# Performance work log

Measured on AMD Instinct MI355X. Metric: run time of the kernel, lower is better.

Reference implementation:

```python
import jax, jax.numpy as jnp
import numpy as np

N_NODES = 384
IN_F = 128
HID = 256
NUM_RBF = 50
NUM_BASIS = 8
NUM_HEADS = 8
HEAD_D = HID // NUM_HEADS
INT_OUT = 2 * NUM_RBF * NUM_BASIS            # K and Q, each num_rbf*num_basis
NODE_OUT = NUM_BASIS * NUM_BASIS + 2 * NUM_BASIS  # W0, B0, W1


def setup_inputs() -> dict:
    key = jax.random.key(0)
    ks = jax.random.split(key, 13)
    s = 0.05
    def p(k, shape):
        return jax.random.normal(k, shape, jnp.float32) * s
    return {
        "h": jax.random.normal(ks[0], (N_NODES, IN_F), jnp.float32),
        "fc_w": p(ks[1], (HID, IN_F)),
        "fc_b": p(ks[2], (HID,)),
        "in_proj_w": p(ks[3], (3 * HID, HID)),
        "in_proj_b": p(ks[4], (3 * HID,)),
        "out_proj_w": p(ks[5], (HID, HID)),
        "out_proj_b": p(ks[6], (HID,)),
        "fci_w1": p(ks[7], (HID, 2 * HID)),
        "fci_b1": p(ks[8], (HID,)),
        "fci_w2": p(ks[9], (INT_OUT, HID)),
        "fci_b2": p(ks[10], (INT_OUT,)),
        "fcn_w": p(ks[11], (NODE_OUT, HID)),
        "fcn_b": p(ks[12], (NODE_OUT,)),
    }


def reference(h, fc_w, fc_b, in_proj_w, in_proj_b, out_proj_w, out_proj_b,
              fci_w1, fci_b1, fci_w2, fci_b2, fcn_w, fcn_b):
    n = h.shape[0]
    # input projection
    h = h @ fc_w.T + fc_b                                   # (n, HID)
    # multihead self-attention (torch nn.MultiheadAttention math)
    qkv = h @ in_proj_w.T + in_proj_b                       # (n, 3*HID)
    q, k, v = jnp.split(qkv, 3, axis=-1)
    def heads(x):
        return x.reshape(n, NUM_HEADS, HEAD_D).transpose(1, 0, 2)  # (H, n, D)
    q, k, v = heads(q), heads(k), heads(v)
    scores = jnp.einsum('hnd,hmd->hnm', q, k) / jnp.sqrt(jnp.asarray(HEAD_D, h.dtype))
    attn = jax.nn.softmax(scores, axis=-1)
    h = jnp.einsum('hnm,hmd->hnd', attn, v).transpose(1, 0, 2).reshape(n, HID)
    h = h @ out_proj_w.T + out_proj_b                       # (n, HID)
    # pairwise interaction: h_interaction[i, j] = concat(h[j], h[i])
    # first Linear split algebraically: cat(hj, hi) @ W1.T = hj@Wa.T + hi@Wb.T
    wa, wb = fci_w1[:, :HID], fci_w1[:, HID:]
    pre = (h @ wa.T)[None, :, :] + (h @ wb.T)[:, None, :] + fci_b1  # (n, n, HID)
    kq = jnp.tanh(pre) @ fci_w2.T + fci_b2                  # (n, n, INT_OUT)
    K, Q = jnp.split(kq, 2, axis=-1)
    K = K.reshape(n, n, NUM_RBF, NUM_BASIS)
    Q = Q.reshape(n, n, NUM_RBF, NUM_BASIS)
    # node-wise parameters
    node = h @ fcn_w.T + fcn_b                              # (n, NODE_OUT)
    b2 = NUM_BASIS * NUM_BASIS
    W0 = node[:, :b2].reshape(n, NUM_BASIS, NUM_BASIS)
    B0 = node[:, b2:b2 + NUM_BASIS]
    W1 = node[:, b2 + NUM_BASIS:].reshape(n, NUM_BASIS, 1)
    return (K, Q, W0, B0, W1)
```

## Files before the change

### kernel.cpp

```cpp
#include <hip/hip_runtime.h>
#include <hip/hip_bf16.h>

typedef __attribute__((ext_vector_type(8))) short bf16x8;
typedef __attribute__((ext_vector_type(4))) float f32x4;

static __device__ __forceinline__ unsigned int f2bf(float f) {
    unsigned int u = __float_as_uint(f);
    u = u + 0x7FFFu + ((u >> 16) & 1u);
    return (u >> 16);
}

static __device__ __forceinline__ float fast_tanh(float x) {
    x = fminf(fmaxf(x, -10.f), 10.f);
    float e = __expf(2.f * x);
    return __fdividef(e - 1.f, e + 1.f);
}

#define LGKM_BAR() do {                                      \
    asm volatile("s_waitcnt lgkmcnt(0)" ::: "memory");       \
    __builtin_amdgcn_s_barrier();                            \
} while (0)

#define LGKM_WAIT() asm volatile("s_waitcnt lgkmcnt(0)" ::: "memory")

__global__ __launch_bounds__(256)
void prep(const float* __restrict__ fc_w, const float* __restrict__ inp_w,
          const float* __restrict__ outp_w, const float* __restrict__ fci_w1,
          const float* __restrict__ fcn_w, const float* __restrict__ fci_w2,
          float* __restrict__ fcwT, float* __restrict__ inpT,
          float* __restrict__ outpT, float* __restrict__ waT,
          float* __restrict__ wbT, float* __restrict__ fcnT,
          uint4* __restrict__ w2p)
{
    const int idx0 = blockIdx.x * 256 + threadIdx.x;
    const int stride = 64 * 256;
    switch (blockIdx.y) {
    case 0:
        for (int c = idx0; c < 32768; c += stride) {
            int k = c >> 8, n = c & 255;
            fcwT[c] = fc_w[n * 128 + k];
        }
        break;
    case 1:
        for (int c = idx0; c < 196608; c += stride) {
            int k = c / 768, n = c - k * 768;
            inpT[c] = inp_w[n * 256 + k];
        }
        break;
    case 2:
        for (int c = idx0; c < 65536; c += stride) {
            int k = c >> 8, n = c & 255;
            outpT[c] = outp_w[n * 256 + k];
        }
        break;
    case 3:
        for (int c = idx0; c < 65536; c += stride) {
            int k = c >> 8, n = c & 255;
            waT[c] = fci_w1[n * 512 + k];
        }
        break;
    case 4:
        for (int c = idx0; c < 65536; c += stride) {
            int k = c >> 8, n = c & 255;
            wbT[c] = fci_w1[n * 512 + 256 + k];
        }
        break;
    case 5:
        for (int c = idx0; c < 20480; c += stride) {
            int k = c / 80, n = c - k * 80;
            fcnT[c] = fcn_w[n * 256 + k];
        }
        break;
    default:
        for (int c = idx0; c < 25600; c += stride) {
            const int n_g = c >> 5, e = c & 31;
            const int kk = e >> 2, kg = e & 3;
            const int ph = (n_g >= 400) ? 1 : 0;
            const int n = n_g - ph * 400;
            const float4* s = (const float4*)(fci_w2 + n_g * 256 + kk * 32 + kg * 8);
            const float4 x0 = s[0], x1 = s[1];
            uint4 pk;
            pk.x = f2bf(x0.x) | (f2bf(x0.y) << 16);
            pk.y = f2bf(x0.z) | (f2bf(x0.w) << 16);
            pk.z = f2bf(x1.x) | (f2bf(x1.y) << 16);
            pk.w = f2bf(x1.z) | (f2bf(x1.w) << 16);
            w2p[((ph * 8 + kk) * 400 + n) * 4 + kg] = pk;
        }
        break;
    }
}

__global__ __launch_bounds__(256)
void k1_rows(const float* __restrict__ h, const float* __restrict__ fc_b,
             const float* __restrict__ inp_b, const float* __restrict__ fcwT,
             const float* __restrict__ inpT, float* __restrict__ qkv)
{
    __shared__ float hrow[128];
    __shared__ float h1row[256];
    const int i = blockIdx.x, part = blockIdx.y, tid = threadIdx.x;
    if (tid < 128) hrow[tid] = h[i * 128 + tid];
    __syncthreads();
    float acc = fc_b[tid];
    #pragma unroll 8
    for (int k = 0; k < 128; ++k) acc += hrow[k] * fcwT[k * 256 + tid];
    h1row[tid] = acc;
    __syncthreads();
    const int col = part * 256 + tid;
    float a = inp_b[col];
    #pragma unroll 8
    for (int k = 0; k < 256; ++k) a += h1row[k] * inpT[k * 768 + col];
    qkv[i * 768 + col] = a;
}

__global__ __launch_bounds__(256)
void attn_kernel(const float* __restrict__ qkv, float* __restrict__ out)
{
    const int n = blockIdx.x;
    const int h = blockIdx.y;
    const int tid = threadIdx.x;
    const int lane = tid & 63;
    const int wid = tid >> 6;

    __shared__ float qs[32];
    __shared__ float p[384];
    __shared__ float red[8];
    __shared__ float pv[8][32];

    if (tid < 32) qs[tid] = qkv[n * 768 + h * 32 + tid] * 0.17677669529663687f;
    __syncthreads();

    float lmax = -1e30f;
    for (int m = tid; m < 384; m += 256) {
        const float4* kr = (const float4*)(qkv + m * 768 + 256 + h * 32);
        float s = 0.f;
        #pragma unroll
        for (int d = 0; d < 8; ++d) {
            float4 kv = kr[d];
            s += qs[d*4+0]*kv.x + qs[d*4+1]*kv.y + qs[d*4+2]*kv.z + qs[d*4+3]*kv.w;
        }
        p[m] = s;
        lmax = fmaxf(lmax, s);
    }
    #pragma unroll
    for (int off = 32; off >= 1; off >>= 1) lmax = fmaxf(lmax, __shfl_xor(lmax, off));
    if (lane == 0) red[wid] = lmax;
    __syncthreads();
    const float gmax = fmaxf(fmaxf(red[0], red[1]), fmaxf(red[2], red[3]));

    float lsum = 0.f;
    for (int m = tid; m < 384; m += 256) {
        float e = __expf(p[m] - gmax);
        p[m] = e;
        lsum += e;
    }
    #pragma unroll
    for (int off = 32; off >= 1; off >>= 1) lsum += __shfl_xor(lsum, off);
    if (lane == 0) red[4 + wid] = lsum;
    __syncthreads();
    const float inv = 1.f / (red[4] + red[5] + red[6] + red[7]);

    const int d = tid & 31;
    const int g = tid >> 5;
    float acc = 0.f;
    for (int m = g * 48; m < g * 48 + 48; ++m)
        acc += p[m] * qkv[m * 768 + 512 + h * 32 + d];
    pv[g][d] = acc;
    __syncthreads();
    if (tid < 32) {
        float o = 0.f;
        #pragma unroll
        for (int gg = 0; gg < 8; ++gg) o += pv[gg][tid];
        out[n * 256 + h * 32 + tid] = o * inv;
    }
}

__global__ __launch_bounds__(256)
void k3_rows(const float* __restrict__ attnO, const float* __restrict__ outp_b,
             const float* __restrict__ fci_b1, const float* __restrict__ fcn_b,
             const float* __restrict__ outpT, const float* __restrict__ waT,
             const float* __restrict__ wbT, const float* __restrict__ fcnT,
             float* __restrict__ hA, float* __restrict__ hB, float* __restrict__ out)
{
    __shared__ float arow[256];
    __shared__ float h2row[256];
    const int i = blockIdx.x, part = blockIdx.y, tid = threadIdx.x;
    arow[tid] = attnO[i * 256 + tid];
    __syncthreads();
    float acc = outp_b[tid];
    #pragma unroll 8
    for (int k = 0; k < 256; ++k) acc += arow[k] * outpT[k * 256 + tid];
    h2row[tid] = acc;
    __syncthreads();
    if (part == 0) {
        float aA = fci_b1[tid];
        #pragma unroll 8
        for (int k = 0; k < 256; ++k) aA += h2row[k] * waT[k * 256 + tid];
        hA[i * 256 + tid] = aA;
    } else if (part == 1) {
        float aB = 0.f;
        #pragma unroll 8
        for (int k = 0; k < 256; ++k) aB += h2row[k] * wbT[k * 256 + tid];
        hB[i * 256 + tid] = aB;
    } else if (tid < 80) {
        float aN = fcn_b[tid];
        #pragma unroll 8
        for (int k = 0; k < 256; ++k) aN += h2row[k] * fcnT[k * 80 + tid];
        if (tid < 64)      out[117964800 + i * 64 + tid] = aN;
        else if (tid < 72) out[117989376 + i * 8 + (tid - 64)] = aN;
        else               out[117992448 + i * 8 + (tid - 72)] = aN;
    }
}

#define CSW_ROWB 336

__global__ __launch_bounds__(320)
void gen_kq(const float* __restrict__ hA, const float* __restrict__ hB,
            const uint4* __restrict__ w2p, const float* __restrict__ b2,
            float* __restrict__ outK, float* __restrict__ outQ)
{
    __shared__ unsigned char Aim[48 * 512];
    __shared__ unsigned char Csw[5][16 * CSW_ROWB];

    const int tid  = threadIdx.x;
    const int lane = tid & 63;
    const int wn   = tid >> 6;
    const int lr   = lane & 15;
    const int kg   = lane >> 4;

    const int bid0 = blockIdx.x;
    const int bid  = (bid0 & 7) * 384 + (bid0 >> 3);

    const int m0  = bid * 48;
    const int ai  = bid >> 3;
    const int bj0 = (bid & 7) * 48;

    for (int c = tid; c < 1536; c += 320) {
        const int row = c >> 5;
        const int e   = c & 31;
        const int ke  = e * 8;
        const float4 a0 = *(const float4*)(hA + (bj0 + row) * 256 + ke);
        const float4 a1 = *(const float4*)(hA + (bj0 + row) * 256 + ke + 4);
        const float4 b0 = *(const float4*)(hB + ai * 256 + ke);
        const float4 b1 = *(const float4*)(hB + ai * 256 + ke + 4);
        uint4 pk;
        pk.x = f2bf(fast_tanh(a0.x + b0.x)) | (f2bf(fast_tanh(a0.y + b0.y)) << 16);
        pk.y = f2bf(fast_tanh(a0.z + b0.z)) | (f2bf(fast_tanh(a0.w + b0.w)) << 16);
        pk.z = f2bf(fast_tanh(a1.x + b1.x)) | (f2bf(fast_tanh(a1.y + b1.y)) << 16);
        pk.w = f2bf(fast_tanh(a1.z + b1.z)) | (f2bf(fast_tanh(a1.w + b1.w)) << 16);
        *(uint4*)(Aim + row * 512 + ((e * 16) ^ ((row & 7) << 4))) = pk;
    }
    LGKM_BAR();

    const int phfirst = bid & 1;
    #pragma unroll
    for (int pp = 0; pp < 2; ++pp) {
        const int ph = pp ^ phfirst;

        f32x4 acc[3][5];
        #pragma unroll
        for (int j = 0; j < 5; ++j) {
            const f32x4 bb = *(const f32x4*)(b2 + ph * 400 + wn * 80 + j * 16 + kg * 4);
            #pragma unroll
            for (int i = 0; i < 3; ++i)
                acc[i][j] = bb;
        }

        #pragma unroll 2
        for (int kk = 0; kk < 8; ++kk) {
            bf16x8 af_[3], bf_[5];
            const uint4* wb = w2p + (ph * 8 + kk) * 1600;
            #pragma unroll
            for (int j = 0; j < 5; ++j)
                bf_[j] = *(const bf16x8*)(wb + (wn * 80 + j * 16 + lr) * 4 + kg);
            #pragma unroll
            for (int i = 0; i < 3; ++i) {
                const int row = i * 16 + lr;
                af_[i] = *(const bf16x8*)(Aim + row * 512 +
                          ((kk * 64 + kg * 16) ^ ((row & 7) << 4)));
            }
            #pragma unroll
            for (int i = 0; i < 3; ++i)
                #pragma unroll
                for (int j = 0; j < 5; ++j)
                    acc[i][j] = __builtin_amdgcn_mfma_f32_16x16x32_bf16(
                        bf_[j], af_[i], acc[i][j], 0, 0, 0);
        }

        float* gob = ph ? outQ : outK;
        unsigned char* slice = Csw[wn];
        #pragma unroll
        for (int i = 0; i < 3; ++i) {
            #pragma unroll
            for (int j = 0; j < 5; ++j)
                *(f32x4*)(slice + lr * CSW_ROWB + (j * 16 + kg * 4) * 4) = acc[i][j];
            LGKM_WAIT();
            float* gb = gob + (size_t)(m0 + i * 16) * 400 + wn * 80;
            #pragma unroll
            for (int q = 0; q < 5; ++q) {
                const int e   = q * 64 + lane;
                const int row = e / 20, c4 = e - row * 20;
                const f32x4 v = *(const f32x4*)(slice + row * CSW_ROWB + c4 * 16);
                *(f32x4*)(gb + row * 400 + c4 * 4) = v;
            }
        }
    }
}

extern "C" void kernel_launch(void* const* d_in, const int* in_sizes, int n_in,
                              void* d_out, int out_size, void* d_ws, size_t ws_size,
                              hipStream_t stream)
{
    (void)in_sizes; (void)n_in; (void)out_size; (void)ws_size;

    const float* h      = (const float*)d_in[0];
    const float* fc_w   = (const float*)d_in[1];
    const float* fc_b   = (const float*)d_in[2];
    const float* inp_w  = (const float*)d_in[3];
    const float* inp_b  = (const float*)d_in[4];
    const float* outp_w = (const float*)d_in[5];
    const float* outp_b = (const float*)d_in[6];
    const float* fci_w1 = (const float*)d_in[7];
    const float* fci_b1 = (const float*)d_in[8];
    const float* fci_w2 = (const float*)d_in[9];
    const float* fci_b2 = (const float*)d_in[10];
    const float* fcn_w  = (const float*)d_in[11];
    const float* fcn_b  = (const float*)d_in[12];

    float* out  = (float*)d_out;
    float* outK = out;
    float* outQ = out + 58982400;

    float* ws    = (float*)d_ws;
    float* qkv   = ws;
    float* attnO = qkv   + 294912;
    float* hA    = attnO + 98304;
    float* hBv   = hA    + 98304;
    float* fcwT  = hBv   + 98304;
    float* inpT  = fcwT  + 32768;
    float* outpT = inpT  + 196608;
    float* waT   = outpT + 65536;
    float* wbT   = waT   + 65536;
    float* fcnT  = wbT   + 65536;
    uint4* w2p   = (uint4*)(fcnT + 20480);

    prep<<<dim3(64, 7), 256, 0, stream>>>(fc_w, inp_w, outp_w, fci_w1, fcn_w, fci_w2,
                                          fcwT, inpT, outpT, waT, wbT, fcnT, w2p);
    k1_rows<<<dim3(384, 3), 256, 0, stream>>>(h, fc_b, inp_b, fcwT, inpT, qkv);
    attn_kernel<<<dim3(384, 8), 256, 0, stream>>>(qkv, attnO);
    k3_rows<<<dim3(384, 3), 256, 0, stream>>>(attnO, outp_b, fci_b1, fcn_b, outpT, waT, wbT, fcnT,
                                              hA, hBv, out);
    gen_kq<<<dim3(3072), 320, 0, stream>>>(hA, hBv, w2p, fci_b2, outK, outQ);
}
```

Measured before the change: 222.1 us.

## Fuse weight prep into k1 and merge attention with output projections

Drops the separate weight-transpose prep kernel, so the small linear layers read the original row-major weights directly, and folds the bf16 packing of fci_w2 into extra blocks of the first kernel. The attention kernel now handles all eight heads for one node per block and also computes the out projection and the fci/fcn projections, cutting five launches down to three and removing the attnO round trip. The trade-off is strided, uncoalesced weight reads per thread, and far fewer blocks (384) in the fused attention stage, each doing serial per-head work.

```diff
diff --git a/kernel.cpp b/kernel.cpp
--- a/kernel.cpp
+++ b/kernel.cpp
@@ -24,55 +24,15 @@
 #define LGKM_WAIT() asm volatile("s_waitcnt lgkmcnt(0)" ::: "memory")
 
 __global__ __launch_bounds__(256)
-void prep(const float* __restrict__ fc_w, const float* __restrict__ inp_w,
-          const float* __restrict__ outp_w, const float* __restrict__ fci_w1,
-          const float* __restrict__ fcn_w, const float* __restrict__ fci_w2,
-          float* __restrict__ fcwT, float* __restrict__ inpT,
-          float* __restrict__ outpT, float* __restrict__ waT,
-          float* __restrict__ wbT, float* __restrict__ fcnT,
-          uint4* __restrict__ w2p)
-{
-    const int idx0 = blockIdx.x * 256 + threadIdx.x;
-    const int stride = 64 * 256;
-    switch (blockIdx.y) {
-    case 0:
-        for (int c = idx0; c < 32768; c += stride) {
-            int k = c >> 8, n = c & 255;
-            fcwT[c] = fc_w[n * 128 + k];
-        }
-        break;
-    case 1:
-        for (int c = idx0; c < 196608; c += stride) {
-            int k = c / 768, n = c - k * 768;
-            inpT[c] = inp_w[n * 256 + k];
-        }
-        break;
-    case 2:
-        for (int c = idx0; c < 65536; c += stride) {
-            int k = c >> 8, n = c & 255;
-            outpT[c] = outp_w[n * 256 + k];
-        }
-        break;
-    case 3:
-        for (int c = idx0; c < 65536; c += stride) {
-            int k = c >> 8, n = c & 255;
-            waT[c] = fci_w1[n * 512 + k];
-        }
-        break;
-    case 4:
-        for (int c = idx0; c < 65536; c += stride) {
-            int k = c >> 8, n = c & 255;
-            wbT[c] = fci_w1[n * 512 + 256 + k];
-        }
-        break;
-    case 5:
-        for (int c = idx0; c < 20480; c += stride) {
-            int k = c / 80, n = c - k * 80;
-            fcnT[c] = fcn_w[n * 256 + k];
-        }
-        break;
-    default:
-        for (int c = idx0; c < 25600; c += stride) {
+void k1_all(const float* __restrict__ h, const float* __restrict__ fc_b,
+            const float* __restrict__ inp_b, const float* __restrict__ fc_w,
+            const float* __restrict__ inp_w, const float* __restrict__ fci_w2,
+            float* __restrict__ qkv, uint4* __restrict__ w2p)
+{
+    const int i = blockIdx.x, part = blockIdx.y, tid = threadIdx.x;
+    if (part == 3) {
+        const int c = i * 256 + tid;
+        if (c < 25600) {
             const int n_g = c >> 5, e = c & 31;
             const int kk = e >> 2, kg = e & 3;
             const int ph = (n_g >= 400) ? 1 : 0;
@@ -86,125 +46,118 @@
             pk.w = f2bf(x1.z) | (f2bf(x1.w) << 16);
             w2p[((ph * 8 + kk) * 400 + n) * 4 + kg] = pk;
         }
-        break;
-    }
-}
-
-__global__ __launch_bounds__(256)
-void k1_rows(const float* __restrict__ h, const float* __restrict__ fc_b,
-             const float* __restrict__ inp_b, const float* __restrict__ fcwT,
-             const float* __restrict__ inpT, float* __restrict__ qkv)
-{
+        return;
+    }
     __shared__ float hrow[128];
     __shared__ float h1row[256];
-    const int i = blockIdx.x, part = blockIdx.y, tid = threadIdx.x;
     if (tid < 128) hrow[tid] = h[i * 128 + tid];
     __syncthreads();
     float acc = fc_b[tid];
-    #pragma unroll 8
-    for (int k = 0; k < 128; ++k) acc += hrow[k] * fcwT[k * 256 + tid];
+    const float* fwr = fc_w + tid * 128;
+    #pragma unroll 8
+    for (int k = 0; k < 128; ++k) acc += hrow[k] * fwr[k];
     h1row[tid] = acc;
     __syncthreads();
     const int col = part * 256 + tid;
     float a = inp_b[col];
-    #pragma unroll 8
-    for (int k = 0; k < 256; ++k) a += h1row[k] * inpT[k * 768 + col];
+    const float* iwr = inp_w + (long)col * 256;
+    #pragma unroll 8
+    for (int k = 0; k < 256; ++k) a += h1row[k] * iwr[k];
     qkv[i * 768 + col] = a;
 }
 
 __global__ __launch_bounds__(256)
-void attn_kernel(const float* __restrict__ qkv, float* __restrict__ out)
-{
-    const int n = blockIdx.x;
-    const int h = blockIdx.y;
+void attn_k3(const float* __restrict__ qkv, const float* __restrict__ outp_b,
+             const float* __restrict__ fci_b1, const float* __restrict__ fcn_b,
+             const float* __restrict__ outp_w, const float* __restrict__ fci_w1,
+             const float* __restrict__ fcn_w,
+             float* __restrict__ hA, float* __restrict__ hB, float* __restrict__ out)
+{
+    const int i = blockIdx.x;
     const int tid = threadIdx.x;
     const int lane = tid & 63;
     const int wid = tid >> 6;
 
-    __shared__ float qs[32];
+    __shared__ float qs[256];
     __shared__ float p[384];
     __shared__ float red[8];
     __shared__ float pv[8][32];
-
-    if (tid < 32) qs[tid] = qkv[n * 768 + h * 32 + tid] * 0.17677669529663687f;
-    __syncthreads();
-
-    float lmax = -1e30f;
-    for (int m = tid; m < 384; m += 256) {
-        const float4* kr = (const float4*)(qkv + m * 768 + 256 + h * 32);
-        float s = 0.f;
-        #pragma unroll
-        for (int d = 0; d < 8; ++d) {
-            float4 kv = kr[d];
-            s += qs[d*4+0]*kv.x + qs[d*4+1]*kv.y + qs[d*4+2]*kv.z + qs[d*4+3]*kv.w;
-        }
-        p[m] = s;
-        lmax = fmaxf(lmax, s);
-    }
-    #pragma unroll
-    for (int off = 32; off >= 1; off >>= 1) lmax = fmaxf(lmax, __shfl_xor(lmax, off));
-    if (lane == 0) red[wid] = lmax;
-    __syncthreads();
-    const float gmax = fmaxf(fmaxf(red[0], red[1]), fmaxf(red[2], red[3]));
-
-    float lsum = 0.f;
-    for (int m = tid; m < 384; m += 256) {
-        float e = __expf(p[m] - gmax);
-        p[m] = e;
-        lsum += e;
-    }
-    #pragma unroll
-    for (int off = 32; off >= 1; off >>= 1) lsum += __shfl_xor(lsum, off);
-    if (lane == 0) red[4 + wid] = lsum;
-    __syncthreads();
-    const float inv = 1.f / (red[4] + red[5] + red[6] + red[7]);
-
-    const int d = tid & 31;
-    const int g = tid >> 5;
-    float acc = 0.f;
-    for (int m = g * 48; m < g * 48 + 48; ++m)
-        acc += p[m] * qkv[m * 768 + 512 + h * 32 + d];
-    pv[g][d] = acc;
-    __syncthreads();
-    if (tid < 32) {
-        float o = 0.f;
-        #pragma unroll
-        for (int gg = 0; gg < 8; ++gg) o += pv[gg][tid];
-        out[n * 256 + h * 32 + tid] = o * inv;
-    }
-}
-
-__global__ __launch_bounds__(256)
-void k3_rows(const float* __restrict__ attnO, const float* __restrict__ outp_b,
-             const float* __restrict__ fci_b1, const float* __restrict__ fcn_b,
-             const float* __restrict__ outpT, const float* __restrict__ waT,
-             const float* __restrict__ wbT, const float* __restrict__ fcnT,
-             float* __restrict__ hA, float* __restrict__ hB, float* __restrict__ out)
-{
     __shared__ float arow[256];
     __shared__ float h2row[256];
-    const int i = blockIdx.x, part = blockIdx.y, tid = threadIdx.x;
-    arow[tid] = attnO[i * 256 + tid];
-    __syncthreads();
+
+    qs[tid] = qkv[i * 768 + tid] * 0.17677669529663687f;
+    __syncthreads();
+
+    for (int hh = 0; hh < 8; ++hh) {
+        float lmax = -1e30f;
+        for (int m = tid; m < 384; m += 256) {
+            const float4* kr = (const float4*)(qkv + m * 768 + 256 + hh * 32);
+            float s = 0.f;
+            #pragma unroll
+            for (int d = 0; d < 8; ++d) {
+                float4 kv = kr[d];
+                s += qs[hh*32+d*4+0]*kv.x + qs[hh*32+d*4+1]*kv.y
+                   + qs[hh*32+d*4+2]*kv.z + qs[hh*32+d*4+3]*kv.w;
+            }
+            p[m] = s;
+            lmax = fmaxf(lmax, s);
+        }
+        #pragma unroll
+        for (int off = 32; off >= 1; off >>= 1) lmax = fmaxf(lmax, __shfl_xor(lmax, off));
+        if (lane == 0) red[wid] = lmax;
+        __syncthreads();
+        const float gmax = fmaxf(fmaxf(red[0], red[1]), fmaxf(red[2], red[3]));
+
+        float lsum = 0.f;
+        for (int m = tid; m < 384; m += 256) {
+            float e = __expf(p[m] - gmax);
+            p[m] = e;
+            lsum += e;
+        }
+        #pragma unroll
+        for (int off = 32; off >= 1; off >>= 1) lsum += __shfl_xor(lsum, off);
+        if (lane == 0) red[4 + wid] = lsum;
+        __syncthreads();
+        const float inv = 1.f / (red[4] + red[5] + red[6] + red[7]);
+
+        const int d = tid & 31;
+        const int g = tid >> 5;
+        float acc = 0.f;
+        for (int m = g * 48; m < g * 48 + 48; ++m)
+            acc += p[m] * qkv[m * 768 + 512 + hh * 32 + d];
+        pv[g][d] = acc;
+        __syncthreads();
+        if (tid < 32) {
+            float o = 0.f;
+            #pragma unroll
+            for (int gg = 0; gg < 8; ++gg) o += pv[gg][tid];
+            arow[hh * 32 + tid] = o * inv;
+        }
+        __syncthreads();
+    }
+
     float acc = outp_b[tid];
-    #pragma unroll 8
-    for (int k = 0; k < 256; ++k) acc += arow[k] * outpT[k * 256 + tid];
+    const float* owr = outp_w + (long)tid * 256;
+    #pragma unroll 8
+    for (int k = 0; k < 256; ++k) acc += arow[k] * owr[k];
     h2row[tid] = acc;
     __syncthreads();
-    if (part == 0) {
-        float aA = fci_b1[tid];
+
+    float aA = fci_b1[tid], aB = 0.f;
+    const float* war = fci_w1 + (long)tid * 512;
+    #pragma unroll 8
+    for (int k = 0; k < 256; ++k) {
+        const float f = h2row[k];
+        aA += f * war[k];
+        aB += f * war[256 + k];
+    }
+    hA[i * 256 + tid] = aA;
+    hB[i * 256 + tid] = aB;
+    if (tid < 80) {
+        float aN = fcn_b[tid];
+        const float* fwr = fcn_w + (long)tid * 256;
         #pragma unroll 8
-        for (int k = 0; k < 256; ++k) aA += h2row[k] * waT[k * 256 + tid];
-        hA[i * 256 + tid] = aA;
-    } else if (part == 1) {
-        float aB = 0.f;
-        #pragma unroll 8
-        for (int k = 0; k < 256; ++k) aB += h2row[k] * wbT[k * 256 + tid];
-        hB[i * 256 + tid] = aB;
-    } else if (tid < 80) {
-        float aN = fcn_b[tid];
-        #pragma unroll 8
-        for (int k = 0; k < 256; ++k) aN += h2row[k] * fcnT[k * 80 + tid];
+        for (int k = 0; k < 256; ++k) aN += h2row[k] * fwr[k];
         if (tid < 64)      out[117964800 + i * 64 + tid] = aN;
         else if (tid < 72) out[117989376 + i * 8 + (tid - 64)] = aN;
         else               out[117992448 + i * 8 + (tid - 72)] = aN;
@@ -332,22 +285,13 @@
 
     float* ws    = (float*)d_ws;
     float* qkv   = ws;
-    float* attnO = qkv   + 294912;
-    float* hA    = attnO + 98304;
-    float* hBv   = hA    + 98304;
-    float* fcwT  = hBv   + 98304;
-    float* inpT  = fcwT  + 32768;
-    float* outpT = inpT  + 196608;
-    float* waT   = outpT + 65536;
-    float* wbT   = waT   + 65536;
-    float* fcnT  = wbT   + 65536;
-    uint4* w2p   = (uint4*)(fcnT + 20480);
-
-    prep<<<dim3(64, 7), 256, 0, stream>>>(fc_w, inp_w, outp_w, fci_w1, fcn_w, fci_w2,
-                                          fcwT, inpT, outpT, waT, wbT, fcnT, w2p);
-    k1_rows<<<dim3(384, 3), 256, 0, stream>>>(h, fc_b, inp_b, fcwT, inpT, qkv);
-    attn_kernel<<<dim3(384, 8), 256, 0, stream>>>(qkv, attnO);
-    k3_rows<<<dim3(384, 3), 256, 0, stream>>>(attnO, outp_b, fci_b1, fcn_b, outpT, waT, wbT, fcnT,
-                                              hA, hBv, out);
+    float* hA    = qkv + 294912;
+    float* hBv   = hA  + 98304;
+    uint4* w2p   = (uint4*)(hBv + 98304);
+
+    k1_all<<<dim3(384, 4), 256, 0, stream>>>(h, fc_b, inp_b, fc_w, inp_w, fci_w2,
+                                             qkv, w2p);
+    attn_k3<<<dim3(384), 256, 0, stream>>>(qkv, outp_b, fci_b1, fcn_b,
+                                           outp_w, fci_w1, fcn_w, hA, hBv, out);
     gen_kq<<<dim3(3072), 320, 0, stream>>>(hA, hBv, w2p, fci_b2, outK, outQ);
 }
```

New measurement: 333.5 us. 1.5x slower.
